# Kernel optimization log

Hardware: AMD Instinct MI355X
Metric: run time of the kernel (lower is better)

Reference implementation:

```python
import jax, jax.numpy as jnp
import numpy as np

N = 50000      # nodes
E = 800000     # edges (before self-loops)
G = 64         # graphs in batch
F_IN = 128
HID = 32
HEADS = 4
OUT = 10
NEG_SLOPE = 0.2  # PyG GATConv default


def setup_inputs() -> dict:
    key = jax.random.key(0)
    ks = jax.random.split(key, 16)
    x = jax.random.normal(ks[0], (N, F_IN), jnp.float32)
    edge_src = jax.random.randint(ks[1], (E,), 0, N)
    edge_dst = jax.random.randint(ks[2], (E,), 0, N)
    batch = jnp.sort(jax.random.randint(ks[3], (N,), 0, G))
    # layer 1: in -> hidden, heads=4, concat
    W1 = jax.random.normal(ks[4], (F_IN, HEADS * HID), jnp.float32) / np.sqrt(F_IN)
    att_src1 = jax.random.normal(ks[5], (HEADS, HID), jnp.float32) / np.sqrt(HID)
    att_dst1 = jax.random.normal(ks[6], (HEADS, HID), jnp.float32) / np.sqrt(HID)
    b1 = jnp.zeros((HEADS * HID,), jnp.float32)
    # layer 2: hidden*heads -> hidden, heads=1
    W2 = jax.random.normal(ks[7], (HEADS * HID, HID), jnp.float32) / np.sqrt(HEADS * HID)
    att_src2 = jax.random.normal(ks[8], (1, HID), jnp.float32) / np.sqrt(HID)
    att_dst2 = jax.random.normal(ks[9], (1, HID), jnp.float32) / np.sqrt(HID)
    b2 = jnp.zeros((HID,), jnp.float32)
    fc_w = jax.random.normal(ks[10], (HID, OUT), jnp.float32) / np.sqrt(HID)
    fc_b = jnp.zeros((OUT,), jnp.float32)
    return dict(x=x, edge_src=edge_src, edge_dst=edge_dst, batch=batch,
                W1=W1, att_src1=att_src1, att_dst1=att_dst1, b1=b1,
                W2=W2, att_src2=att_src2, att_dst2=att_dst2, b2=b2,
                fc_w=fc_w, fc_b=fc_b)


def gat_conv(x, si, di, W, a_src, a_dst, b):
    n = x.shape[0]
    H, C = a_src.shape
    h = (x @ W).reshape(n, H, C)                    # [N,H,C]
    alpha_src = jnp.sum(h * a_src, axis=-1)         # [N,H]
    alpha_dst = jnp.sum(h * a_dst, axis=-1)         # [N,H]
    logits = jax.nn.leaky_relu(alpha_src[si] + alpha_dst[di], NEG_SLOPE)  # [Et,H]
    # segment softmax grouped by destination node (self-loops => no empty segments)
    m = jax.ops.segment_max(logits, di, num_segments=n)
    e = jnp.exp(logits - m[di])
    denom = jax.ops.segment_sum(e, di, num_segments=n)
    alpha = e / denom[di]                           # [Et,H]
    out = jax.ops.segment_sum(alpha[:, :, None] * h[si], di, num_segments=n)
    return out.reshape(n, H * C) + b


def reference(x, edge_src, edge_dst, batch,
              W1, att_src1, att_dst1, b1,
              W2, att_src2, att_dst2, b2,
              fc_w, fc_b):
    n = x.shape[0]
    loops = jnp.arange(n)
    si = jnp.concatenate([edge_src, loops])   # PyG add_self_loops=True
    di = jnp.concatenate([edge_dst, loops])
    h = gat_conv(x, si, di, W1, att_src1, att_dst1, b1)
    h = jax.nn.relu(h)                         # dropout identity (eval)
    h = gat_conv(h, si, di, W2, att_src2, att_dst2, b2)
    h = jax.nn.relu(h)
    # global mean pool over graphs
    sums = jax.ops.segment_sum(h, batch, num_segments=G)
    cnt = jax.ops.segment_sum(jnp.ones((n,), h.dtype), batch, num_segments=G)
    pooled = sums / jnp.maximum(cnt, 1.0)[:, None]
    return pooled @ fc_w + fc_b
```

## Files before the change

### kernel.cpp

```cpp
#include <hip/hip_runtime.h>
#include <hip/hip_fp16.h>

#define NEG_SLOPE 0.2f
#define GN 64
#define OUTC 10
#define EPB 4096
#define NPB 512
#define REC_CAP 9984

typedef _Float16 f16x8 __attribute__((ext_vector_type(8)));
typedef float f32x4 __attribute__((ext_vector_type(4)));

__device__ __forceinline__ float lrelu(float x) { return x > 0.f ? x : NEG_SLOPE * x; }

__global__ __launch_bounds__(256) void k_parta_prep(
    const int* __restrict__ di, int* __restrict__ blkcnt, int E, int nb, int nblk,
    const float* __restrict__ W1, const float* __restrict__ W2,
    __half* __restrict__ W1T, __half* __restrict__ W2T)
{
    int t = threadIdx.x;
    if (blockIdx.x >= nblk) {
        int t0 = (blockIdx.x - nblk) * 256 + t;
        for (int i = t0; i < 128 * 128; i += 16 * 256) {
            int k = i >> 7, n = i & 127;
            W1T[n * 128 + k] = __float2half_rn(W1[i]);
        }
        for (int i = t0; i < 128 * 32; i += 16 * 256) {
            int k = i >> 5, n = i & 31;
            W2T[n * 128 + k] = __float2half_rn(W2[i]);
        }
        return;
    }
    __shared__ int lcnt[128];
    for (int i = t; i < nb; i += 256) lcnt[i] = 0;
    __syncthreads();
    int base = blockIdx.x * EPB;
    #pragma unroll
    for (int k = 0; k < 16; ++k) {
        int e = base + t + k * 256;
        if (e < E) atomicAdd(&lcnt[di[e] >> 9], 1);
    }
    __syncthreads();
    for (int i = t; i < nb; i += 256) blkcnt[blockIdx.x * nb + i] = lcnt[i];
}

__global__ __launch_bounds__(256) void k_colscan(
    const int* __restrict__ blkcnt, int* __restrict__ blkbase,
    int* __restrict__ bsum, int nblk, int nb)
{
    __shared__ int s[256];
    int b = blockIdx.x, t = threadIdx.x;
    int v = (t < nblk) ? blkcnt[t * nb + b] : 0;
    s[t] = v;
    __syncthreads();
    for (int off = 1; off < 256; off <<= 1) {
        int u = (t >= off) ? s[t - off] : 0;
        __syncthreads();
        s[t] += u;
        __syncthreads();
    }
    if (t < nblk) blkbase[t * nb + b] = s[t] - v;
    if (t == 255) bsum[b] = s[255];
}

__global__ __launch_bounds__(256) void k_parta2_gemm1(
    const int* __restrict__ si, const int* __restrict__ di,
    const int* __restrict__ blkbase, const int* __restrict__ bsum,
    unsigned* __restrict__ rec, int* __restrict__ recbase, int E, int nb, int nblk,
    const float* __restrict__ x, const __half* __restrict__ W1T,
    const float* __restrict__ asrc, const float* __restrict__ adst,
    __half* __restrict__ h1, float* __restrict__ as1, float* __restrict__ ad1, int N)
{
    __shared__ int smem[384];
    if (blockIdx.x >= nblk) {
        int blk = blockIdx.x - nblk;
        int wave = threadIdx.x >> 6, lane = threadIdx.x & 63;
        int row0 = blk * 64 + wave * 16;
        int ar = row0 + (lane & 15);
        int arc = min(ar, N - 1);
        int k0 = (lane >> 4) * 8;
        const float* xr = x + (size_t)arc * 128 + k0;
        f16x8 afrag[4];
        #pragma unroll
        for (int kk = 0; kk < 4; ++kk) {
            float4 u0 = *(const float4*)(xr + kk * 32);
            float4 u1 = *(const float4*)(xr + kk * 32 + 4);
            f16x8 a;
            a[0] = (_Float16)u0.x; a[1] = (_Float16)u0.y;
            a[2] = (_Float16)u0.z; a[3] = (_Float16)u0.w;
            a[4] = (_Float16)u1.x; a[5] = (_Float16)u1.y;
            a[6] = (_Float16)u1.z; a[7] = (_Float16)u1.w;
            afrag[kk] = a;
        }
        int cl = lane & 15;
        int rbase = row0 + 4 * (lane >> 4);
        const _Float16* WT = (const _Float16*)W1T;
        float ps[4][4] = {};
        float pd[4][4] = {};
        #pragma unroll
        for (int t = 0; t < 8; ++t) {
            int col = t * 16 + cl;
            float av = asrc[col];
            float dv = adst[col];
            const _Float16* wrow = WT + (size_t)col * 128 + k0;
            f32x4 acc = {0.f, 0.f, 0.f, 0.f};
            #pragma unroll
            for (int kk = 0; kk < 4; ++kk) {
                f16x8 b = *(const f16x8*)(wrow + kk * 32);
                acc = __builtin_amdgcn_mfma_f32_16x16x32_f16(afrag[kk], b, acc, 0, 0, 0);
            }
            int h = t >> 1;
            #pragma unroll
            for (int r = 0; r < 4; ++r) {
                ps[r][h] += acc[r] * av;
                pd[r][h] += acc[r] * dv;
                int row = rbase + r;
                if (row < N)
                    h1[(size_t)row * 128 + col] = __float2half_rn(acc[r]);
            }
        }
        #pragma unroll
        for (int r = 0; r < 4; ++r)
            #pragma unroll
            for (int h = 0; h < 4; ++h) {
                float a = ps[r][h], b = pd[r][h];
                #pragma unroll
                for (int m = 1; m < 16; m <<= 1) {
                    a += __shfl_xor(a, m);
                    b += __shfl_xor(b, m);
                }
                ps[r][h] = a; pd[r][h] = b;
            }
        if (cl == 0) {
            #pragma unroll
            for (int r = 0; r < 4; ++r) {
                int row = rbase + r;
                if (row < N) {
                    ((float4*)as1)[row] = make_float4(ps[r][0], ps[r][1], ps[r][2], ps[r][3]);
                    ((float4*)ad1)[row] = make_float4(pd[r][0], pd[r][1], pd[r][2], pd[r][3]);
                }
            }
        }
        return;
    }

    int* ls    = smem;
    int* lbase = smem + 128;
    int* lcnt  = smem + 256;
    int t = threadIdx.x;
    int v = 0;
    if (t < 128) {
        v = (t < nb) ? bsum[t] : 0;
        ls[t] = v;
    }
    __syncthreads();
    for (int off = 1; off < 128; off <<= 1) {
        int u = (t < 128 && t >= off) ? ls[t - off] : 0;
        __syncthreads();
        if (t < 128) ls[t] += u;
        __syncthreads();
    }
    if (t < 128) {
        lbase[t] = (ls[t] - v) + ((t < nb) ? blkbase[blockIdx.x * nb + t] : 0);
        lcnt[t] = 0;
    }
    if (blockIdx.x == 0 && t < nb) recbase[t] = ls[t] - v;
    __syncthreads();
    int base = blockIdx.x * EPB;
    #pragma unroll
    for (int k = 0; k < 16; ++k) {
        int e = base + t + k * 256;
        if (e < E) {
            int d = di[e];
            int b = d >> 9;
            int r = atomicAdd(&lcnt[b], 1);
            rec[lbase[b] + r] = ((unsigned)(d & 511) << 17) | (unsigned)si[e];
        }
    }
}

__global__ __launch_bounds__(512) void k_partb(
    const unsigned* __restrict__ rec, const int* __restrict__ bsum,
    const int* __restrict__ recbase,
    int* __restrict__ csr_src, int* __restrict__ row_start,
    int* __restrict__ deg, int N, int nb)
{
    __shared__ int lhist[512], lexcl[512], lcur[512];
    __shared__ unsigned lsrc[REC_CAP];
    int b = blockIdx.x, t = threadIdx.x;
    int n0 = b << 9;
    int nn = min(512, N - n0);
    int gb = recbase[b];
    int S = bsum[b];
    if (S > REC_CAP) S = REC_CAP;
    lhist[t] = 0;
    __syncthreads();
    for (int i = t; i < S; i += 512)
        atomicAdd(&lhist[rec[gb + i] >> 17], 1);
    __syncthreads();
    int v = lhist[t];
    lexcl[t] = v;
    __syncthreads();
    for (int off = 1; off < 512; off <<= 1) {
        int u = (t >= off) ? lexcl[t - off] : 0;
        __syncthreads();
        lexcl[t] += u;
        __syncthreads();
    }
    int excl = lexcl[t] - v;
    __syncthreads();
    lexcl[t] = excl;
    lcur[t] = excl;
    __syncthreads();
    for (int i = t; i < S; i += 512) {
        unsigned r = rec[gb + i];
        int p = atomicAdd(&lcur[r >> 17], 1);
        if (p < REC_CAP) lsrc[p] = r & 0x1FFFFu;
    }
    __syncthreads();
    for (int i = t; i < S; i += 512) csr_src[gb + i] = (int)lsrc[i];
    if (t < nn) {
        deg[n0 + t] = lhist[t];
        row_start[n0 + t] = gb + lexcl[t];
    }
}

__global__ __launch_bounds__(256) void k_agg1(
    const int* __restrict__ csr_src, const int* __restrict__ row_start,
    const int* __restrict__ deg,
    const __half* __restrict__ h1, const float* __restrict__ as1,
    const float* __restrict__ ad1, __half* __restrict__ out1, int N)
{
    int idx = blockIdx.x * 256 + threadIdx.x;
    int node = idx >> 4, lane = idx & 15;
    if (node >= N) return;
    int head = lane >> 2;
    const float4* h16 = (const float4*)h1;
    float ad = ad1[4 * node + head];
    float m0 = lrelu(as1[4 * node + head] + ad);
    float den = 1.f;
    float acc[8];
    {
        float4 raw = h16[(size_t)node * 16 + lane];
        const __half2* hh = (const __half2*)&raw;
        #pragma unroll
        for (int q = 0; q < 4; ++q) {
            float2 f = __half22float2(hh[q]);
            acc[2 * q] = f.x; acc[2 * q + 1] = f.y;
        }
    }

    int e0 = row_start[node];
    int d  = deg[node];
    int nbatch = (d + 7) >> 3;

    auto LOAD = [&](int t, int s[8], float4 r[8], float& w0, float& w1) {
        int base = e0 + t * 8;
        int last = e0 + d;
        #pragma unroll
        for (int j = 0; j < 8; ++j) {
            int ix = base + j;
            s[j] = csr_src[ix < last ? ix : e0];
        }
        #pragma unroll
        for (int j = 0; j < 8; ++j) r[j] = h16[(size_t)s[j] * 16 + lane];
        int j0 = (lane & 3) * 2;
        float a0 = as1[4 * s[j0] + head];
        float a1 = as1[4 * s[j0 + 1] + head];
        w0 = __expf(lrelu(a0 + ad) - m0);
        w1 = __expf(lrelu(a1 + ad) - m0);
    };
    auto CONSUME = [&](int t, const int s[8], const float4 r[8], float w0, float w1) {
        int rem = d - t * 8;
        #pragma unroll
        for (int j = 0; j < 8; ++j) {
            int srcl = (lane & 12) | (j >> 1);
            float w = __shfl((j & 1) ? w1 : w0, srcl, 16);
            w = (j < rem) ? w : 0.f;
            den += w;
            const __half2* hh = (const __half2*)&r[j];
            #pragma unroll
            for (int q = 0; q < 4; ++q) {
                float2 g = __half22float2(hh[q]);
                acc[2 * q]     += w * g.x;
                acc[2 * q + 1] += w * g.y;
            }
        }
    };

    if (nbatch > 0) {
        int sA[8]; float4 rA[8]; float wA0, wA1;
        LOAD(0, sA, rA, wA0, wA1);
        for (int t = 0; t < nbatch - 1; ++t) {
            int sB[8]; float4 rB[8]; float wB0, wB1;
            LOAD(t + 1, sB, rB, wB0, wB1);
            CONSUME(t, sA, rA, wA0, wA1);
            #pragma unroll
            for (int j = 0; j < 8; ++j) { sA[j] = sB[j]; rA[j] = rB[j]; }
            wA0 = wB0; wA1 = wB1;
        }
        CONSUME(nbatch - 1, sA, rA, wA0, wA1);
    }

    float inv = 1.f / den;
    __half2 o[4];
    #pragma unroll
    for (int q = 0; q < 4; ++q)
        o[q] = __floats2half2_rn(acc[2 * q] * inv, acc[2 * q + 1] * inv);
    ((float4*)out1)[(size_t)node * 16 + lane] = *(float4*)o;
}

__global__ __launch_bounds__(256) void k_gemm2(
    const __half* __restrict__ out1h, const float* __restrict__ b1,
    const __half* __restrict__ W2T, const float* __restrict__ asrc2,
    const float* __restrict__ adst2, __half* __restrict__ h2,
    float* __restrict__ as2, float* __restrict__ ad2, int N)
{
    int wave = threadIdx.x >> 6, lane = threadIdx.x & 63;
    int row0 = blockIdx.x * 64 + wave * 16;
    int ar = row0 + (lane & 15);
    int arc = min(ar, N - 1);
    int k0 = (lane >> 4) * 8;
    const __half* xr = out1h + (size_t)arc * 128 + k0;
    const float* br = b1 + k0;
    f16x8 afrag[4];
    #pragma unroll
    for (int kk = 0; kk < 4; ++kk) {
        float4 raw = *(const float4*)(xr + kk * 32);
        const __half2* hh = (const __half2*)&raw;
        float4 c0 = *(const float4*)(br + kk * 32);
        float4 c1 = *(const float4*)(br + kk * 32 + 4);
        float bb[8] = {c0.x, c0.y, c0.z, c0.w, c1.x, c1.y, c1.z, c1.w};
        f16x8 a;
        #pragma unroll
        for (int j = 0; j < 4; ++j) {
            float2 f = __half22float2(hh[j]);
            a[2 * j]     = (_Float16)fmaxf(f.x + bb[2 * j], 0.f);
            a[2 * j + 1] = (_Float16)fmaxf(f.y + bb[2 * j + 1], 0.f);
        }
        afrag[kk] = a;
    }
    int cl = lane & 15;
    int rbase = row0 + 4 * (lane >> 4);
    const _Float16* WT = (const _Float16*)W2T;
    float ps[4] = {}, pd[4] = {};
    #pragma unroll
    for (int t = 0; t < 2; ++t) {
        int col = t * 16 + cl;
        float av = asrc2[col];
        float dv = adst2[col];
        const _Float16* wrow = WT + (size_t)col * 128 + k0;
        f32x4 acc = {0.f, 0.f, 0.f, 0.f};
        #pragma unroll
        for (int kk = 0; kk < 4; ++kk) {
            f16x8 b = *(const f16x8*)(wrow + kk * 32);
            acc = __builtin_amdgcn_mfma_f32_16x16x32_f16(afrag[kk], b, acc, 0, 0, 0);
        }
        #pragma unroll
        for (int r = 0; r < 4; ++r) {
            ps[r] += acc[r] * av;
            pd[r] += acc[r] * dv;
            int row = rbase + r;
            if (row < N)
                h2[(size_t)row * 32 + col] = __float2half_rn(acc[r]);
        }
    }
    #pragma unroll
    for (int r = 0; r < 4; ++r) {
        float a = ps[r], b = pd[r];
        #pragma unroll
        for (int m = 1; m < 16; m <<= 1) {
            a += __shfl_xor(a, m);
            b += __shfl_xor(b, m);
        }
        if (cl == 0) {
            int row = rbase + r;
            if (row < N) { as2[row] = a; ad2[row] = b; }
        }
    }
}

__global__ __launch_bounds__(256) void k_agg2(
    const int* __restrict__ csr_src, const int* __restrict__ row_start,
    const int* __restrict__ deg,
    const __half* __restrict__ h2, const float* __restrict__ as2,
    const float* __restrict__ ad2, __half* __restrict__ out2, int N)
{
    int idx = blockIdx.x * 256 + threadIdx.x;
    int node = idx >> 3, lane = idx & 7;
    if (node >= N) return;
    const float2* hv = (const float2*)h2;
    float ad = ad2[node];
    float m0 = lrelu(as2[node] + ad);
    float den = 1.f;
    float acc[4];
    {
        float2 raw = hv[(size_t)node * 8 + lane];
        const __half2* hh = (const __half2*)&raw;
        float2 f0 = __half22float2(hh[0]);
        float2 f1 = __half22float2(hh[1]);
        acc[0] = f0.x; acc[1] = f0.y; acc[2] = f1.x; acc[3] = f1.y;
    }

    int e0 = row_start[node];
    int d  = deg[node];
    int nbatch = (d + 7) >> 3;

    auto LOAD = [&](int t, int s[8], float2 r[8], float& wv) {
        int base = e0 + t * 8;
        int last = e0 + d;
        #pragma unroll
        for (int j = 0; j < 8; ++j) {
            int ix = base + j;
            s[j] = csr_src[ix < last ? ix : e0];
        }
        #pragma unroll
        for (int j = 0; j < 8; ++j) r[j] = hv[(size_t)s[j] * 8 + lane];
        float a = as2[s[lane]];
        wv = __expf(lrelu(a + ad) - m0);
    };
    auto CONSUME = [&](int t, const int s[8], const float2 r[8], float wv) {
        int rem = d - t * 8;
        #pragma unroll
        for (int j = 0; j < 8; ++j) {
            float w = __shfl(wv, j, 8);
            w = (j < rem) ? w : 0.f;
            den += w;
            const __half2* hh = (const __half2*)&r[j];
            float2 g0 = __half22float2(hh[0]);
            float2 g1 = __half22float2(hh[1]);
            acc[0] += w * g0.x; acc[1] += w * g0.y;
            acc[2] += w * g1.x; acc[3] += w * g1.y;
        }
    };

    if (nbatch > 0) {
        int sA[8]; float2 rA[8]; float wA;
        LOAD(0, sA, rA, wA);
        for (int t = 0; t < nbatch - 1; ++t) {
            int sB[8]; float2 rB[8]; float wB;
            LOAD(t + 1, sB, rB, wB);
            CONSUME(t, sA, rA, wA);
            #pragma unroll
            for (int j = 0; j < 8; ++j) { sA[j] = sB[j]; rA[j] = rB[j]; }
            wA = wB;
        }
        CONSUME(nbatch - 1, sA, rA, wA);
    }

    float inv = 1.f / den;
    __half2 o0 = __floats2half2_rn(acc[0] * inv, acc[1] * inv);
    __half2 o1 = __floats2half2_rn(acc[2] * inv, acc[3] * inv);
    float2 pk;
    *(__half2*)&pk.x = o0;
    *(__half2*)&pk.y = o1;
    ((float2*)out2)[(size_t)node * 8 + lane] = pk;
}

__global__ __launch_bounds__(256) void k_pool(
    const __half* __restrict__ out2, const float* __restrict__ b2,
    const int* __restrict__ batch, float* __restrict__ partial, int N)
{
    int g = blockIdx.x >> 2, chunkid = blockIdx.x & 3;
    int lo = 0, hi = N;
    while (lo < hi) { int mid = (lo + hi) >> 1; if (batch[mid] < g) lo = mid + 1; else hi = mid; }
    int start = lo;
    hi = N;
    while (lo < hi) { int mid = (lo + hi) >> 1; if (batch[mid] < g + 1) lo = mid + 1; else hi = mid; }
    int end = lo;
    int len = end - start;
    int chunk = (len + 3) >> 2;
    int s0 = start + chunkid * chunk;
    int s1 = min(s0 + chunk, end);

    int tid = threadIdx.x;
    int c = tid & 31, r = tid >> 5;
    float bias = b2[c];
    float acc = 0.f;
    for (int i = s0 + r; i < s1; i += 8)
        acc += fmaxf(__half2float(out2[(size_t)i * 32 + c]) + bias, 0.f);
    __shared__ float s[8][32];
    s[r][c] = acc;
    __syncthreads();
    if (r == 0) {
        float v = s[0][c] + s[1][c] + s[2][c] + s[3][c] +
                  s[4][c] + s[5][c] + s[6][c] + s[7][c];
        partial[(size_t)blockIdx.x * 32 + c] = v;
    }
}

__global__ __launch_bounds__(256) void k_fc(
    const float* __restrict__ partial, const int* __restrict__ batch,
    const float* __restrict__ fc_w, const float* __restrict__ fc_b,
    float* __restrict__ out, int N)
{
    __shared__ float pooled[GN][32];
    __shared__ float cnts[GN];
    int t = threadIdx.x;
    for (int idx = t; idx < GN * 32; idx += 256) {
        int g = idx >> 5, c = idx & 31;
        pooled[g][c] = partial[(g * 4 + 0) * 32 + c] + partial[(g * 4 + 1) * 32 + c] +
                       partial[(g * 4 + 2) * 32 + c] + partial[(g * 4 + 3) * 32 + c];
    }
    if (t < GN) {
        int g = t;
        int lo = 0, hi = N;
        while (lo < hi) { int mid = (lo + hi) >> 1; if (batch[mid] < g) lo = mid + 1; else hi = mid; }
        int start = lo;
        hi = N;
        while (lo < hi) { int mid = (lo + hi) >> 1; if (batch[mid] < g + 1) lo = mid + 1; else hi = mid; }
        cnts[g] = fmaxf((float)(lo - start), 1.f);
    }
    __syncthreads();
    for (int idx = t; idx < GN * OUTC; idx += 256) {
        int g = idx / OUTC, o = idx % OUTC;
        float inv = 1.f / cnts[g];
        float a = fc_b[o];
        #pragma unroll
        for (int c = 0; c < 32; ++c)
            a += pooled[g][c] * inv * fc_w[c * OUTC + o];
        out[idx] = a;
    }
}

extern "C" void kernel_launch(void* const* d_in, const int* in_sizes, int n_in,
                              void* d_out, int out_size, void* d_ws, size_t ws_size,
                              hipStream_t stream)
{
    const float* x        = (const float*)d_in[0];
    const int*   esrc     = (const int*)d_in[1];
    const int*   edst     = (const int*)d_in[2];
    const int*   batch    = (const int*)d_in[3];
    const float* W1       = (const float*)d_in[4];
    const float* att_src1 = (const float*)d_in[5];
    const float* att_dst1 = (const float*)d_in[6];
    const float* b1       = (const float*)d_in[7];
    const float* W2       = (const float*)d_in[8];
    const float* att_src2 = (const float*)d_in[9];
    const float* att_dst2 = (const float*)d_in[10];
    const float* b2       = (const float*)d_in[11];
    const float* fc_w     = (const float*)d_in[12];
    const float* fc_b     = (const float*)d_in[13];
    int N = in_sizes[3];
    int E = in_sizes[1];
    float* out = (float*)d_out;

    int nb   = (N + NPB - 1) >> 9;
    int nblk = (E + EPB - 1) / EPB;

    float*    base  = (float*)d_ws;
    __half*   h1    = (__half*)base;
    float*    as1   = base + (size_t)N * 64;
    float*    ad1   = as1 + (size_t)N * 4;
    __half*   out1  = (__half*)(ad1 + (size_t)N * 4);
    __half*   h2    = (__half*)(ad1 + (size_t)N * 4 + (size_t)N * 64);
    float*    as2   = ad1 + (size_t)N * 4 + (size_t)N * 64 + (size_t)N * 16;
    float*    ad2   = as2 + N;
    __half*   out2  = (__half*)(ad2 + N);
    float*    partial = ad2 + N + (size_t)N * 16;
    int*      deg       = (int*)(partial + GN * 4 * 32);
    int*      row_start = deg + N;
    int*      csr_src   = row_start + N;
    unsigned* rec       = (unsigned*)(csr_src + E);
    int*      blkcnt    = (int*)(rec + E);
    int*      blkbase   = blkcnt + (size_t)nblk * nb;
    int*      bsum      = blkbase + (size_t)nblk * nb;
    int*      recbase   = bsum + nb;
    __half*   W1T       = (__half*)(recbase + nb);
    __half*   W2T       = W1T + 128 * 128;

    int nb_row = (N + 63) / 64;

    k_parta_prep<<<nblk + 16, 256, 0, stream>>>(edst, blkcnt, E, nb, nblk, W1, W2, W1T, W2T);
    k_colscan<<<nb, 256, 0, stream>>>(blkcnt, blkbase, bsum, nblk, nb);
    k_parta2_gemm1<<<nblk + nb_row, 256, 0, stream>>>(
        esrc, edst, blkbase, bsum, rec, recbase, E, nb, nblk,
        x, W1T, att_src1, att_dst1, h1, as1, ad1, N);
    k_partb<<<nb, 512, 0, stream>>>(rec, bsum, recbase, csr_src, row_start, deg, N, nb);

    k_agg1<<<(N * 16 + 255) / 256, 256, 0, stream>>>(csr_src, row_start, deg, h1, as1, ad1, out1, N);

    k_gemm2<<<nb_row, 256, 0, stream>>>(out1, b1, W2T, att_src2, att_dst2, h2, as2, ad2, N);
    k_agg2<<<(N * 8 + 255) / 256, 256, 0, stream>>>(csr_src, row_start, deg, h2, as2, ad2, out2, N);

    k_pool<<<GN * 4, 256, 0, stream>>>(out2, b2, batch, partial, N);
    k_fc  <<<1, 256, 0, stream>>>(partial, batch, fc_w, fc_b, out, N);
}
```

Measured before the change: 136.6 us.

## Fuse layer-2 linear transform and attention scores into layer-1 aggregation kernel

Removes the separate k_gemm2 kernel and the out1 intermediate buffer by doing the bias+ReLU, 128x32 projection, and attention-score reductions inside k_agg1. Each 16-lane node group broadcasts its 128 activations via shuffles and computes two output columns per lane with scalar FMAs against W2T staged in LDS. This saves a launch and the write and re-read of N*128 half values, at the cost of replacing MFMA with scalar FP32 math, adding an LDS staging step and a sync to every agg1 block, and increasing register pressure in a latency-bound gather kernel.

```diff
diff --git a/kernel.cpp b/kernel.cpp
--- a/kernel.cpp
+++ b/kernel.cpp
@@ -229,8 +229,22 @@
     const int* __restrict__ csr_src, const int* __restrict__ row_start,
     const int* __restrict__ deg,
     const __half* __restrict__ h1, const float* __restrict__ as1,
-    const float* __restrict__ ad1, __half* __restrict__ out1, int N)
-{
+    const float* __restrict__ ad1, const float* __restrict__ b1,
+    const __half* __restrict__ W2T, const float* __restrict__ asrc2,
+    const float* __restrict__ adst2, __half* __restrict__ h2,
+    float* __restrict__ as2, float* __restrict__ ad2, int N)
+{
+    __shared__ __half w2s[32 * 132];
+    {
+        int t = threadIdx.x;
+        for (int i = t; i < 32 * 16; i += 256) {
+            int c = i >> 4, ch = i & 15;
+            *(float4*)(w2s + c * 132 + ch * 8) =
+                *(const float4*)(W2T + c * 128 + ch * 8);
+        }
+    }
+    __syncthreads();
+
     int idx = blockIdx.x * 256 + threadIdx.x;
     int node = idx >> 4, lane = idx & 15;
     if (node >= N) return;
@@ -303,81 +317,49 @@
     }
 
     float inv = 1.f / den;
-    __half2 o[4];
+    float4 bv0 = *(const float4*)(b1 + lane * 8);
+    float4 bv1 = *(const float4*)(b1 + lane * 8 + 4);
+    float x2r[8];
+    x2r[0] = fmaxf(acc[0] * inv + bv0.x, 0.f);
+    x2r[1] = fmaxf(acc[1] * inv + bv0.y, 0.f);
+    x2r[2] = fmaxf(acc[2] * inv + bv0.z, 0.f);
+    x2r[3] = fmaxf(acc[3] * inv + bv0.w, 0.f);
+    x2r[4] = fmaxf(acc[4] * inv + bv1.x, 0.f);
+    x2r[5] = fmaxf(acc[5] * inv + bv1.y, 0.f);
+    x2r[6] = fmaxf(acc[6] * inv + bv1.z, 0.f);
+    x2r[7] = fmaxf(acc[7] * inv + bv1.w, 0.f);
+
+    int c0 = 2 * lane;
+    const __half2* wr0 = (const __half2*)(w2s + c0 * 132);
+    const __half2* wr1 = (const __half2*)(w2s + (c0 + 1) * 132);
+    float s0a = 0.f, s0b = 0.f, s1a = 0.f, s1b = 0.f;
+    for (int src = 0; src < 16; ++src) {
+        float xv[8];
+        #pragma unroll
+        for (int j = 0; j < 8; ++j) xv[j] = __shfl(x2r[j], src, 16);
+        #pragma unroll
+        for (int p = 0; p < 4; ++p) {
+            float2 w0f = __half22float2(wr0[src * 4 + p]);
+            float2 w1f = __half22float2(wr1[src * 4 + p]);
+            if (p & 1) {
+                s0b += xv[2*p] * w0f.x + xv[2*p+1] * w0f.y;
+                s1b += xv[2*p] * w1f.x + xv[2*p+1] * w1f.y;
+            } else {
+                s0a += xv[2*p] * w0f.x + xv[2*p+1] * w0f.y;
+                s1a += xv[2*p] * w1f.x + xv[2*p+1] * w1f.y;
+            }
+        }
+    }
+    float s0 = s0a + s0b, s1 = s1a + s1b;
+    ((__half2*)h2)[(size_t)node * 16 + lane] = __floats2half2_rn(s0, s1);
+    float pa = s0 * asrc2[c0] + s1 * asrc2[c0 + 1];
+    float pb = s0 * adst2[c0] + s1 * adst2[c0 + 1];
     #pragma unroll
-    for (int q = 0; q < 4; ++q)
-        o[q] = __floats2half2_rn(acc[2 * q] * inv, acc[2 * q + 1] * inv);
-    ((float4*)out1)[(size_t)node * 16 + lane] = *(float4*)o;
-}
-
-__global__ __launch_bounds__(256) void k_gemm2(
-    const __half* __restrict__ out1h, const float* __restrict__ b1,
-    const __half* __restrict__ W2T, const float* __restrict__ asrc2,
-    const float* __restrict__ adst2, __half* __restrict__ h2,
-    float* __restrict__ as2, float* __restrict__ ad2, int N)
-{
-    int wave = threadIdx.x >> 6, lane = threadIdx.x & 63;
-    int row0 = blockIdx.x * 64 + wave * 16;
-    int ar = row0 + (lane & 15);
-    int arc = min(ar, N - 1);
-    int k0 = (lane >> 4) * 8;
-    const __half* xr = out1h + (size_t)arc * 128 + k0;
-    const float* br = b1 + k0;
-    f16x8 afrag[4];
-    #pragma unroll
-    for (int kk = 0; kk < 4; ++kk) {
-        float4 raw = *(const float4*)(xr + kk * 32);
-        const __half2* hh = (const __half2*)&raw;
-        float4 c0 = *(const float4*)(br + kk * 32);
-        float4 c1 = *(const float4*)(br + kk * 32 + 4);
-        float bb[8] = {c0.x, c0.y, c0.z, c0.w, c1.x, c1.y, c1.z, c1.w};
-        f16x8 a;
-        #pragma unroll
-        for (int j = 0; j < 4; ++j) {
-            float2 f = __half22float2(hh[j]);
-            a[2 * j]     = (_Float16)fmaxf(f.x + bb[2 * j], 0.f);
-            a[2 * j + 1] = (_Float16)fmaxf(f.y + bb[2 * j + 1], 0.f);
-        }
-        afrag[kk] = a;
-    }
-    int cl = lane & 15;
-    int rbase = row0 + 4 * (lane >> 4);
-    const _Float16* WT = (const _Float16*)W2T;
-    float ps[4] = {}, pd[4] = {};
-    #pragma unroll
-    for (int t = 0; t < 2; ++t) {
-        int col = t * 16 + cl;
-        float av = asrc2[col];
-        float dv = adst2[col];
-        const _Float16* wrow = WT + (size_t)col * 128 + k0;
-        f32x4 acc = {0.f, 0.f, 0.f, 0.f};
-        #pragma unroll
-        for (int kk = 0; kk < 4; ++kk) {
-            f16x8 b = *(const f16x8*)(wrow + kk * 32);
-            acc = __builtin_amdgcn_mfma_f32_16x16x32_f16(afrag[kk], b, acc, 0, 0, 0);
-        }
-        #pragma unroll
-        for (int r = 0; r < 4; ++r) {
-            ps[r] += acc[r] * av;
-            pd[r] += acc[r] * dv;
-            int row = rbase + r;
-            if (row < N)
-                h2[(size_t)row * 32 + col] = __float2half_rn(acc[r]);
-        }
-    }
-    #pragma unroll
-    for (int r = 0; r < 4; ++r) {
-        float a = ps[r], b = pd[r];
-        #pragma unroll
-        for (int m = 1; m < 16; m <<= 1) {
-            a += __shfl_xor(a, m);
-            b += __shfl_xor(b, m);
-        }
-        if (cl == 0) {
-            int row = rbase + r;
-            if (row < N) { as2[row] = a; ad2[row] = b; }
-        }
-    }
+    for (int m = 1; m < 16; m <<= 1) {
+        pa += __shfl_xor(pa, m);
+        pb += __shfl_xor(pb, m);
+    }
+    if (lane == 0) { as2[node] = pa; ad2[node] = pb; }
 }
 
 __global__ __launch_bounds__(256) void k_agg2(
@@ -552,9 +534,8 @@
     __half*   h1    = (__half*)base;
     float*    as1   = base + (size_t)N * 64;
     float*    ad1   = as1 + (size_t)N * 4;
-    __half*   out1  = (__half*)(ad1 + (size_t)N * 4);
-    __half*   h2    = (__half*)(ad1 + (size_t)N * 4 + (size_t)N * 64);
-    float*    as2   = ad1 + (size_t)N * 4 + (size_t)N * 64 + (size_t)N * 16;
+    __half*   h2    = (__half*)(ad1 + (size_t)N * 4);
+    float*    as2   = ad1 + (size_t)N * 4 + (size_t)N * 16;
     float*    ad2   = as2 + N;
     __half*   out2  = (__half*)(ad2 + N);
     float*    partial = ad2 + N + (size_t)N * 16;
@@ -578,9 +559,10 @@
         x, W1T, att_src1, att_dst1, h1, as1, ad1, N);
     k_partb<<<nb, 512, 0, stream>>>(rec, bsum, recbase, csr_src, row_start, deg, N, nb);
 
-    k_agg1<<<(N * 16 + 255) / 256, 256, 0, stream>>>(csr_src, row_start, deg, h1, as1, ad1, out1, N);
-
-    k_gemm2<<<nb_row, 256, 0, stream>>>(out1, b1, W2T, att_src2, att_dst2, h2, as2, ad2, N);
+    k_agg1<<<(N * 16 + 255) / 256, 256, 0, stream>>>(
+        csr_src, row_start, deg, h1, as1, ad1,
+        b1, W2T, att_src2, att_dst2, h2, as2, ad2, N);
+
     k_agg2<<<(N * 8 + 255) / 256, 256, 0, stream>>>(csr_src, row_start, deg, h2, as2, ad2, out2, N);
 
     k_pool<<<GN * 4, 256, 0, stream>>>(out2, b2, batch, partial, N);
```

Measured after the change: 135.9 us. Within noise of the previous version (-0.5%).

## Fuse layer-2 aggregation with global mean pooling via shared-memory bins and atomics

Applied to the files above, without the earlier changes.

The second-layer aggregation kernel now applies bias and ReLU itself and accumulates each node's result into per-graph bins in shared memory. The bins are then flushed with global atomics into a zeroed pool buffer. This removes the out2 write and re-read and the separate pool kernel launch, at the cost of an added memset and atomic contention. Float atomics also make the summation order nondeterministic.

```diff
diff --git a/kernel.cpp b/kernel.cpp
--- a/kernel.cpp
+++ b/kernel.cpp
@@ -380,30 +380,40 @@
     }
 }
 
-__global__ __launch_bounds__(256) void k_agg2(
+__global__ __launch_bounds__(256) void k_agg2pool(
     const int* __restrict__ csr_src, const int* __restrict__ row_start,
     const int* __restrict__ deg,
     const __half* __restrict__ h2, const float* __restrict__ as2,
-    const float* __restrict__ ad2, __half* __restrict__ out2, int N)
-{
-    int idx = blockIdx.x * 256 + threadIdx.x;
-    int node = idx >> 3, lane = idx & 7;
-    if (node >= N) return;
+    const float* __restrict__ ad2, const float* __restrict__ b2,
+    const int* __restrict__ batch, float* __restrict__ pool, int N)
+{
+    __shared__ float lbin[32][33];
+    int tid = threadIdx.x;
+    for (int i = tid; i < 32 * 33; i += 256) ((float*)lbin)[i] = 0.f;
+    __syncthreads();
+
+    int node0 = blockIdx.x * 32;
+    int node  = node0 + (tid >> 3);
+    int lane  = tid & 7;
+    bool valid = node < N;
+    int nc = min(node, N - 1);
+    int gmin = batch[min(node0, N - 1)];
+
     const float2* hv = (const float2*)h2;
-    float ad = ad2[node];
-    float m0 = lrelu(as2[node] + ad);
+    float ad = ad2[nc];
+    float m0 = lrelu(as2[nc] + ad);
     float den = 1.f;
     float acc[4];
     {
-        float2 raw = hv[(size_t)node * 8 + lane];
+        float2 raw = hv[(size_t)nc * 8 + lane];
         const __half2* hh = (const __half2*)&raw;
         float2 f0 = __half22float2(hh[0]);
         float2 f1 = __half22float2(hh[1]);
         acc[0] = f0.x; acc[1] = f0.y; acc[2] = f1.x; acc[3] = f1.y;
     }
 
-    int e0 = row_start[node];
-    int d  = deg[node];
+    int e0 = row_start[nc];
+    int d  = deg[nc];
     int nbatch = (d + 7) >> 3;
 
     auto LOAD = [&](int t, int s[8], float2 r[8], float& wv) {
@@ -449,48 +459,29 @@
     }
 
     float inv = 1.f / den;
-    __half2 o0 = __floats2half2_rn(acc[0] * inv, acc[1] * inv);
-    __half2 o1 = __floats2half2_rn(acc[2] * inv, acc[3] * inv);
-    float2 pk;
-    *(__half2*)&pk.x = o0;
-    *(__half2*)&pk.y = o1;
-    ((float2*)out2)[(size_t)node * 8 + lane] = pk;
-}
-
-__global__ __launch_bounds__(256) void k_pool(
-    const __half* __restrict__ out2, const float* __restrict__ b2,
-    const int* __restrict__ batch, float* __restrict__ partial, int N)
-{
-    int g = blockIdx.x >> 2, chunkid = blockIdx.x & 3;
-    int lo = 0, hi = N;
-    while (lo < hi) { int mid = (lo + hi) >> 1; if (batch[mid] < g) lo = mid + 1; else hi = mid; }
-    int start = lo;
-    hi = N;
-    while (lo < hi) { int mid = (lo + hi) >> 1; if (batch[mid] < g + 1) lo = mid + 1; else hi = mid; }
-    int end = lo;
-    int len = end - start;
-    int chunk = (len + 3) >> 2;
-    int s0 = start + chunkid * chunk;
-    int s1 = min(s0 + chunk, end);
-
-    int tid = threadIdx.x;
-    int c = tid & 31, r = tid >> 5;
-    float bias = b2[c];
-    float acc = 0.f;
-    for (int i = s0 + r; i < s1; i += 8)
-        acc += fmaxf(__half2float(out2[(size_t)i * 32 + c]) + bias, 0.f);
-    __shared__ float s[8][32];
-    s[r][c] = acc;
-    __syncthreads();
-    if (r == 0) {
-        float v = s[0][c] + s[1][c] + s[2][c] + s[3][c] +
-                  s[4][c] + s[5][c] + s[6][c] + s[7][c];
-        partial[(size_t)blockIdx.x * 32 + c] = v;
+    int c0 = 4 * lane;
+    int gl = min(batch[nc] - gmin, 31);
+    __half2 q0 = __floats2half2_rn(acc[0] * inv, acc[1] * inv);
+    __half2 q1 = __floats2half2_rn(acc[2] * inv, acc[3] * inv);
+    float2 v0 = __half22float2(q0);
+    float2 v1 = __half22float2(q1);
+    if (valid) {
+        atomicAdd(&lbin[gl][c0 + 0], fmaxf(v0.x + b2[c0 + 0], 0.f));
+        atomicAdd(&lbin[gl][c0 + 1], fmaxf(v0.y + b2[c0 + 1], 0.f));
+        atomicAdd(&lbin[gl][c0 + 2], fmaxf(v1.x + b2[c0 + 2], 0.f));
+        atomicAdd(&lbin[gl][c0 + 3], fmaxf(v1.y + b2[c0 + 3], 0.f));
+    }
+    __syncthreads();
+    int glast = min(batch[min(node0 + 31, N - 1)] - gmin, 31);
+    for (int t = tid; t < (glast + 1) * 32; t += 256) {
+        int gl2 = t >> 5, c = t & 31;
+        float v = lbin[gl2][c];
+        if (v != 0.f) atomicAdd(&pool[(gmin + gl2) * 32 + c], v);
     }
 }
 
 __global__ __launch_bounds__(256) void k_fc(
-    const float* __restrict__ partial, const int* __restrict__ batch,
+    const float* __restrict__ pool, const int* __restrict__ batch,
     const float* __restrict__ fc_w, const float* __restrict__ fc_b,
     float* __restrict__ out, int N)
 {
@@ -499,8 +490,7 @@
     int t = threadIdx.x;
     for (int idx = t; idx < GN * 32; idx += 256) {
         int g = idx >> 5, c = idx & 31;
-        pooled[g][c] = partial[(g * 4 + 0) * 32 + c] + partial[(g * 4 + 1) * 32 + c] +
-                       partial[(g * 4 + 2) * 32 + c] + partial[(g * 4 + 3) * 32 + c];
+        pooled[g][c] = pool[g * 32 + c];
     }
     if (t < GN) {
         int g = t;
@@ -556,9 +546,8 @@
     __half*   h2    = (__half*)(ad1 + (size_t)N * 4 + (size_t)N * 64);
     float*    as2   = ad1 + (size_t)N * 4 + (size_t)N * 64 + (size_t)N * 16;
     float*    ad2   = as2 + N;
-    __half*   out2  = (__half*)(ad2 + N);
-    float*    partial = ad2 + N + (size_t)N * 16;
-    int*      deg       = (int*)(partial + GN * 4 * 32);
+    float*    pool  = ad2 + N;
+    int*      deg       = (int*)(pool + GN * 32);
     int*      row_start = deg + N;
     int*      csr_src   = row_start + N;
     unsigned* rec       = (unsigned*)(csr_src + E);
@@ -571,6 +560,8 @@
 
     int nb_row = (N + 63) / 64;
 
+    hipMemsetAsync(pool, 0, GN * 32 * sizeof(float), stream);
+
     k_parta_prep<<<nblk + 16, 256, 0, stream>>>(edst, blkcnt, E, nb, nblk, W1, W2, W1T, W2T);
     k_colscan<<<nb, 256, 0, stream>>>(blkcnt, blkbase, bsum, nblk, nb);
     k_parta2_gemm1<<<nblk + nb_row, 256, 0, stream>>>(
@@ -581,8 +572,9 @@
     k_agg1<<<(N * 16 + 255) / 256, 256, 0, stream>>>(csr_src, row_start, deg, h1, as1, ad1, out1, N);
 
     k_gemm2<<<nb_row, 256, 0, stream>>>(out1, b1, W2T, att_src2, att_dst2, h2, as2, ad2, N);
-    k_agg2<<<(N * 8 + 255) / 256, 256, 0, stream>>>(csr_src, row_start, deg, h2, as2, ad2, out2, N);
-
-    k_pool<<<GN * 4, 256, 0, stream>>>(out2, b2, batch, partial, N);
-    k_fc  <<<1, 256, 0, stream>>>(partial, batch, fc_w, fc_b, out, N);
-}
+
+    k_agg2pool<<<(N * 8 + 255) / 256, 256, 0, stream>>>(
+        csr_src, row_start, deg, h2, as2, ad2, b2, batch, pool, N);
+
+    k_fc<<<1, 256, 0, stream>>>(pool, batch, fc_w, fc_b, out, N);
+}
```

Measured after the change: 131.8 us. -3.5%, faster.
